# Kernel tuning notes

Measured on AMD Instinct MI355X. Metric: run time of the kernel, lower is better.

The kernel has to match this reference:

```python
import jax, jax.numpy as jnp
import numpy as np

N_NODES = 100000
N_EDGES = 600000
IN_CH = 128
HID = 128


def setup_inputs() -> dict:
    key = jax.random.key(0)
    ks = jax.random.split(key, 8)
    x = jax.random.normal(ks[0], (N_NODES, IN_CH), dtype=jnp.float32)
    edge_index = jax.random.randint(ks[1], (2, N_EDGES), 0, N_NODES, dtype=jnp.int64)
    # Linear weights stored as (in, out); scaled like torch default init
    W1 = jax.random.normal(ks[2], (2 * IN_CH, HID), dtype=jnp.float32) / np.sqrt(2 * IN_CH)
    b1 = jnp.zeros((HID,), dtype=jnp.float32)
    W2 = jax.random.normal(ks[3], (HID, HID), dtype=jnp.float32) / np.sqrt(HID)
    b2 = jnp.zeros((HID,), dtype=jnp.float32)
    W3 = jax.random.normal(ks[4], (HID, 1), dtype=jnp.float32) / np.sqrt(HID)
    b3 = jnp.zeros((1,), dtype=jnp.float32)
    return {"x": x, "edge_index": edge_index, "W1": W1, "b1": b1,
            "W2": W2, "b2": b2, "W3": W3, "b3": b3}


def reference(x, edge_index, W1, b1, W2, b2, W3, b3):
    src = edge_index[0]
    tgt = edge_index[1]
    # gather + concat: [n_edges, 2*in_channels]
    h = jnp.concatenate([x[src, :], x[tgt, :]], axis=1)
    h = jax.nn.elu(h @ W1 + b1)
    h = jax.nn.elu(h @ W2 + b2)
    h = h @ W3 + b3  # [n_edges, 1]
    return jnp.squeeze(h)  # squeeze=True path -> [n_edges]
```

## Files before the change

kernel.cpp:

```cpp
#include <hip/hip_runtime.h>

#define N_NODES 100000
#define N_EDGES 600000
#define NT1 1563
#define NT2 9375
#define LDH 136
typedef _Float16 f16x8 __attribute__((ext_vector_type(8)));
typedef __attribute__((ext_vector_type(4))) float f32x4;

__device__ __forceinline__ float elu_f(float v) {
    return v > 0.0f ? v : (__expf(v) - 1.0f);
}

extern "C" __global__ __launch_bounds__(256)
void k0_w1f(const float* __restrict__ W1, _Float16* __restrict__ W1f) {
    const int t = threadIdx.x;
    const int id = blockIdx.x * 256 + t;
    const int lane = id & 63, f = id >> 6;
    const int ks = f & 3, c = (f >> 2) & 1, half = (f >> 3) & 1, w = f >> 4;
    const int ln = lane & 15, kg = lane >> 4;
    const int col = w * 32 + c * 16 + ln;
    f16x8 v;
#pragma unroll
    for (int j = 0; j < 8; ++j)
        v[j] = (_Float16)W1[(half * 128 + ks * 32 + kg * 8 + j) * 128 + col];
    *(f16x8*)(W1f + (size_t)id * 8) = v;
}

extern "C" __global__ __launch_bounds__(256, 3)
void k1_node_linear(const float* __restrict__ x, const _Float16* __restrict__ W1f,
                    _Float16* __restrict__ P) {
    __shared__ __align__(16) _Float16 sX[64 * LDH];

    const int t = threadIdx.x;
    const int w = t >> 6, lane = t & 63;
    const int ln = lane & 15, kg = lane >> 4;
    const int le = t >> 2;
    const int q  = t & 3;

    f16x8 bf[2][2][4];
#pragma unroll
    for (int half = 0; half < 2; ++half)
#pragma unroll
        for (int c = 0; c < 2; ++c)
#pragma unroll
            for (int ks = 0; ks < 4; ++ks)
                bf[half][c][ks] = *(const f16x8*)(
                    W1f + (size_t)((w * 16 + half * 8 + c * 4 + ks) * 64 + lane) * 8);

    for (int tile = blockIdx.x; tile < NT1; tile += gridDim.x) {
        const int n0 = tile * 64;
        __syncthreads();

        {
            int n = n0 + le;
#pragma unroll
            for (int i = 0; i < 4; ++i) {
                float4 a0 = make_float4(0.f, 0.f, 0.f, 0.f), a1 = a0;
                if (n < N_NODES) {
                    const float* p = x + (size_t)n * 128 + q * 32 + i * 8;
                    a0 = *(const float4*)p; a1 = *(const float4*)(p + 4);
                }
                f16x8 vh;
                vh[0] = (_Float16)a0.x; vh[1] = (_Float16)a0.y;
                vh[2] = (_Float16)a0.z; vh[3] = (_Float16)a0.w;
                vh[4] = (_Float16)a1.x; vh[5] = (_Float16)a1.y;
                vh[6] = (_Float16)a1.z; vh[7] = (_Float16)a1.w;
                *(f16x8*)(&sX[le * LDH + q * 32 + i * 8]) = vh;
            }
        }
        __syncthreads();

        f32x4 acc[2][4][2];
#pragma unroll
        for (int half = 0; half < 2; ++half)
#pragma unroll
            for (int rt = 0; rt < 4; ++rt)
#pragma unroll
                for (int c = 0; c < 2; ++c) acc[half][rt][c] = (f32x4){0.f, 0.f, 0.f, 0.f};

#pragma unroll
        for (int ks = 0; ks < 4; ++ks) {
#pragma unroll
            for (int rt = 0; rt < 4; ++rt) {
                f16x8 a = *(const f16x8*)(&sX[(rt * 16 + ln) * LDH + ks * 32 + kg * 8]);
#pragma unroll
                for (int half = 0; half < 2; ++half)
#pragma unroll
                    for (int c = 0; c < 2; ++c)
                        acc[half][rt][c] = __builtin_amdgcn_mfma_f32_16x16x32_f16(
                            a, bf[half][c][ks], acc[half][rt][c], 0, 0, 0);
            }
        }

#pragma unroll
        for (int half = 0; half < 2; ++half) {
            __syncthreads();
#pragma unroll
            for (int rt = 0; rt < 4; ++rt)
#pragma unroll
                for (int c = 0; c < 2; ++c) {
                    int col = w * 32 + c * 16 + ln;
#pragma unroll
                    for (int reg = 0; reg < 4; ++reg) {
                        int row = rt * 16 + kg * 4 + reg;
                        sX[row * LDH + col] = (_Float16)acc[half][rt][c][reg];
                    }
                }
            __syncthreads();
            int n = n0 + le;
            if (n < N_NODES) {
                _Float16* dst = P + (size_t)n * 256 + half * 128 + q * 32;
                const _Float16* srcp = &sX[le * LDH + q * 32];
#pragma unroll
                for (int i = 0; i < 4; ++i)
                    *(f16x8*)(dst + i * 8) = *(const f16x8*)(srcp + i * 8);
            }
        }
    }
}

extern "C" __global__ __launch_bounds__(256, 3)
void k2_edge_mlp(const _Float16* __restrict__ P, const void* __restrict__ eiv,
                 const float* __restrict__ b1, const float* __restrict__ W2,
                 const float* __restrict__ b2, const float* __restrict__ W3,
                 const float* __restrict__ b3, float* __restrict__ out) {
    __shared__ __align__(16) _Float16 sH[2][64 * LDH];
    __shared__ float sPart[2][4][64];
    __shared__ int sFlag;

    const int t = threadIdx.x;
    const int w = t >> 6, lane = t & 63;
    const int ln = lane & 15, kg = lane >> 4;
    const int row = t >> 2;
    const int kc0 = (t & 3) * 4;
    const float b3v = b3[0];
    const int stride = gridDim.x;

    if (t < 64) {
        unsigned v = ((const unsigned*)eiv)[2 * t + 1];
        unsigned long long bm = __ballot(v == 0u);
        if (t == 0) sFlag = (bm == ~0ull) ? 1 : 0;
    }

    f16x8 b1f[4];
#pragma unroll
    for (int i = 0; i < 4; ++i)
#pragma unroll
        for (int j = 0; j < 8; ++j) b1f[i][j] = (_Float16)b1[(kc0 + i) * 8 + j];

    float w3v[2], b2v[2];
#pragma unroll
    for (int c = 0; c < 2; ++c) {
        int col = w * 32 + c * 16 + ln;
        w3v[c] = W3[col]; b2v[c] = b2[col];
    }

    f16x8 bfw[2][4];
#pragma unroll
    for (int c = 0; c < 2; ++c) {
        const int n = w * 32 + c * 16 + ln;
#pragma unroll
        for (int ks = 0; ks < 4; ++ks) {
            f16x8 v;
#pragma unroll
            for (int j = 0; j < 8; ++j) {
                int k = ks * 32 + kg * 8 + j;
                v[j] = (_Float16)W2[k * 128 + n];
            }
            bfw[c][ks] = v;
        }
    }
    __syncthreads();
    const int mode64 = sFlag;

    const int tile0 = blockIdx.x;

    int se_nx, ge_nx;
    {
        int e = tile0 * 64 + row;
        if (mode64) {
            se_nx = (int)((const long long*)eiv)[e];
            ge_nx = (int)((const long long*)eiv)[N_EDGES + e];
        } else {
            se_nx = ((const int*)eiv)[e];
            ge_nx = ((const int*)eiv)[N_EDGES + e];
        }
    }
    {
        const _Float16* pa = P + (size_t)se_nx * 256 + kc0 * 8;
        const _Float16* pb = P + (size_t)ge_nx * 256 + 128 + kc0 * 8;
        f16x8 Ga[4], Gb[4];
#pragma unroll
        for (int i = 0; i < 4; ++i) {
            Ga[i] = *(const f16x8*)(pa + i * 8);
            Gb[i] = *(const f16x8*)(pb + i * 8);
        }
#pragma unroll
        for (int i = 0; i < 4; ++i) {
            f16x8 s = Ga[i] + Gb[i] + b1f[i];
            f16x8 vh;
#pragma unroll
            for (int j = 0; j < 8; ++j) {
                _Float16 sv = s[j];
                vh[j] = (sv > (_Float16)0) ? sv
                        : (_Float16)(__expf((float)sv) - 1.0f);
            }
            *(f16x8*)(&sH[0][row * LDH + (kc0 + i) * 8]) = vh;
        }
    }
    {
        int t1 = tile0 + stride;
        int t1c = (t1 < NT2) ? t1 : tile0;
        int e = t1c * 64 + row;
        if (mode64) {
            se_nx = (int)((const long long*)eiv)[e];
            ge_nx = (int)((const long long*)eiv)[N_EDGES + e];
        } else {
            se_nx = ((const int*)eiv)[e];
            ge_nx = ((const int*)eiv)[N_EDGES + e];
        }
    }
    __syncthreads();

    int p = 0;
    int prevE0 = -1;
    for (int tile = tile0; tile < NT2; tile += stride) {
        const int nt = tile + stride;
        const int ntc = (nt < NT2) ? nt : tile;

        const _Float16* pa = P + (size_t)se_nx * 256 + kc0 * 8;
        const _Float16* pb = P + (size_t)ge_nx * 256 + 128 + kc0 * 8;
        f16x8 Ga[4], Gb[4];
#pragma unroll
        for (int i = 0; i < 4; ++i) {
            Ga[i] = *(const f16x8*)(pa + i * 8);
            Gb[i] = *(const f16x8*)(pb + i * 8);
        }

        {
            int n2 = nt + stride;
            int n2c = (n2 < NT2) ? n2 : ntc;
            int e = n2c * 64 + row;
            if (mode64) {
                se_nx = (int)((const long long*)eiv)[e];
                ge_nx = (int)((const long long*)eiv)[N_EDGES + e];
            } else {
                se_nx = ((const int*)eiv)[e];
                ge_nx = ((const int*)eiv)[N_EDGES + e];
            }
        }

        if (prevE0 >= 0 && t < 64)
            out[prevE0 + t] = sPart[p ^ 1][0][t] + sPart[p ^ 1][1][t] +
                              sPart[p ^ 1][2][t] + sPart[p ^ 1][3][t] + b3v;

        f32x4 acc[4][2];
#pragma unroll
        for (int rt = 0; rt < 4; ++rt)
#pragma unroll
            for (int c = 0; c < 2; ++c) acc[rt][c] = (f32x4){0.f, 0.f, 0.f, 0.f};

#pragma unroll
        for (int ks = 0; ks < 4; ++ks) {
#pragma unroll
            for (int rt = 0; rt < 4; ++rt) {
                f16x8 a = *(const f16x8*)(&sH[p][(rt * 16 + ln) * LDH + ks * 32 + kg * 8]);
#pragma unroll
                for (int c = 0; c < 2; ++c)
                    acc[rt][c] = __builtin_amdgcn_mfma_f32_16x16x32_f16(a, bfw[c][ks], acc[rt][c], 0, 0, 0);
            }
        }

#pragma unroll
        for (int rt = 0; rt < 4; ++rt) {
            float pr[4] = {0.f, 0.f, 0.f, 0.f};
#pragma unroll
            for (int c = 0; c < 2; ++c) {
#pragma unroll
                for (int reg = 0; reg < 4; ++reg)
                    pr[reg] += elu_f(acc[rt][c][reg] + b2v[c]) * w3v[c];
            }
#pragma unroll
            for (int m = 1; m < 16; m <<= 1)
#pragma unroll
                for (int reg = 0; reg < 4; ++reg) pr[reg] += __shfl_xor(pr[reg], m, 64);
            if (ln == 0) {
#pragma unroll
                for (int reg = 0; reg < 4; ++reg)
                    sPart[p][w][rt * 16 + kg * 4 + reg] = pr[reg];
            }
        }

#pragma unroll
        for (int i = 0; i < 4; ++i) {
            f16x8 s = Ga[i] + Gb[i] + b1f[i];
            f16x8 vh;
#pragma unroll
            for (int j = 0; j < 8; ++j) {
                _Float16 sv = s[j];
                vh[j] = (sv > (_Float16)0) ? sv
                        : (_Float16)(__expf((float)sv) - 1.0f);
            }
            *(f16x8*)(&sH[p ^ 1][row * LDH + (kc0 + i) * 8]) = vh;
        }

        prevE0 = tile * 64;
        __syncthreads();
        p ^= 1;
    }

    if (prevE0 >= 0 && t < 64)
        out[prevE0 + t] = sPart[p ^ 1][0][t] + sPart[p ^ 1][1][t] +
                          sPart[p ^ 1][2][t] + sPart[p ^ 1][3][t] + b3v;
}

extern "C" void kernel_launch(void* const* d_in, const int* in_sizes, int n_in,
                              void* d_out, int out_size, void* d_ws, size_t ws_size,
                              hipStream_t stream) {
    const float* x  = (const float*)d_in[0];
    const void*  ei = d_in[1];
    const float* W1 = (const float*)d_in[2];
    const float* b1 = (const float*)d_in[3];
    const float* W2 = (const float*)d_in[4];
    const float* b2 = (const float*)d_in[5];
    const float* W3 = (const float*)d_in[6];
    const float* b3 = (const float*)d_in[7];
    float* out = (float*)d_out;

    _Float16* P   = (_Float16*)((char*)d_ws + 256);
    _Float16* W1f = P + (size_t)N_NODES * 256;

    k0_w1f<<<16, 256, 0, stream>>>(W1, W1f);
    k1_node_linear<<<768, 256, 0, stream>>>(x, W1f, P);
    k2_edge_mlp<<<768, 256, 0, stream>>>(P, ei, b1, W2, b2, W3, b3, out);
}
```

Before: 192.1 us.

## Prefetch gathered node rows one tile ahead via register double buffer

Moves the gather of the source and target node rows for tile t+1 into iteration t, and loads edge indices two tiles ahead instead of one. The rows are held in a second register buffer and rotated at the end of each iteration. The aim is to hide the latency of the random global gathers behind the MFMA and ELU work of the current tile. In exchange it costs about 32 more VGPRs, which may lower occupancy. The prologue index loads for tile0+stride and tile0+2*stride are not clamped against the tile count.

New measurement: 240.0 us. 25.0% more time.

```diff
diff --git a/kernel.cpp b/kernel.cpp
--- a/kernel.cpp
+++ b/kernel.cpp
@@ -176,20 +176,22 @@
 
     const int tile0 = blockIdx.x;
 
-    int se_nx, ge_nx;
+#define LOAD_IDX(TT, SE, GE) do {                                   \
+        int e_ = (TT) * 64 + row;                                   \
+        if (mode64) {                                               \
+            SE = (int)((const long long*)eiv)[e_];                  \
+            GE = (int)((const long long*)eiv)[N_EDGES + e_];        \
+        } else {                                                    \
+            SE = ((const int*)eiv)[e_];                             \
+            GE = ((const int*)eiv)[N_EDGES + e_];                   \
+        }                                                           \
+    } while (0)
+
     {
-        int e = tile0 * 64 + row;
-        if (mode64) {
-            se_nx = (int)((const long long*)eiv)[e];
-            ge_nx = (int)((const long long*)eiv)[N_EDGES + e];
-        } else {
-            se_nx = ((const int*)eiv)[e];
-            ge_nx = ((const int*)eiv)[N_EDGES + e];
-        }
-    }
-    {
-        const _Float16* pa = P + (size_t)se_nx * 256 + kc0 * 8;
-        const _Float16* pb = P + (size_t)ge_nx * 256 + 128 + kc0 * 8;
+        int se, ge;
+        LOAD_IDX(tile0, se, ge);
+        const _Float16* pa = P + (size_t)se * 256 + kc0 * 8;
+        const _Float16* pb = P + (size_t)ge * 256 + 128 + kc0 * 8;
         f16x8 Ga[4], Gb[4];
 #pragma unroll
         for (int i = 0; i < 4; ++i) {
@@ -209,46 +211,40 @@
             *(f16x8*)(&sH[0][row * LDH + (kc0 + i) * 8]) = vh;
         }
     }
+    f16x8 GaA[4], GbA[4];
     {
-        int t1 = tile0 + stride;
-        int t1c = (t1 < NT2) ? t1 : tile0;
-        int e = t1c * 64 + row;
-        if (mode64) {
-            se_nx = (int)((const long long*)eiv)[e];
-            ge_nx = (int)((const long long*)eiv)[N_EDGES + e];
-        } else {
-            se_nx = ((const int*)eiv)[e];
-            ge_nx = ((const int*)eiv)[N_EDGES + e];
-        }
-    }
+        int se, ge;
+        LOAD_IDX(tile0 + stride, se, ge);
+        const _Float16* pa = P + (size_t)se * 256 + kc0 * 8;
+        const _Float16* pb = P + (size_t)ge * 256 + 128 + kc0 * 8;
+#pragma unroll
+        for (int i = 0; i < 4; ++i) {
+            GaA[i] = *(const f16x8*)(pa + i * 8);
+            GbA[i] = *(const f16x8*)(pb + i * 8);
+        }
+    }
+    int se_nx, ge_nx;
+    LOAD_IDX(tile0 + 2 * stride, se_nx, ge_nx);
     __syncthreads();
 
     int p = 0;
     int prevE0 = -1;
     for (int tile = tile0; tile < NT2; tile += stride) {
-        const int nt = tile + stride;
-        const int ntc = (nt < NT2) ? nt : tile;
-
-        const _Float16* pa = P + (size_t)se_nx * 256 + kc0 * 8;
-        const _Float16* pb = P + (size_t)ge_nx * 256 + 128 + kc0 * 8;
-        f16x8 Ga[4], Gb[4];
-#pragma unroll
-        for (int i = 0; i < 4; ++i) {
-            Ga[i] = *(const f16x8*)(pa + i * 8);
-            Gb[i] = *(const f16x8*)(pb + i * 8);
-        }
-
+        f16x8 GaB[4], GbB[4];
         {
-            int n2 = nt + stride;
-            int n2c = (n2 < NT2) ? n2 : ntc;
-            int e = n2c * 64 + row;
-            if (mode64) {
-                se_nx = (int)((const long long*)eiv)[e];
-                ge_nx = (int)((const long long*)eiv)[N_EDGES + e];
-            } else {
-                se_nx = ((const int*)eiv)[e];
-                ge_nx = ((const int*)eiv)[N_EDGES + e];
-            }
+            const _Float16* pa = P + (size_t)se_nx * 256 + kc0 * 8;
+            const _Float16* pb = P + (size_t)ge_nx * 256 + 128 + kc0 * 8;
+#pragma unroll
+            for (int i = 0; i < 4; ++i) {
+                GaB[i] = *(const f16x8*)(pa + i * 8);
+                GbB[i] = *(const f16x8*)(pb + i * 8);
+            }
+        }
+
+        {
+            int n3 = tile + 3 * stride;
+            int n3c = (n3 < NT2) ? n3 : tile;
+            LOAD_IDX(n3c, se_nx, ge_nx);
         }
 
         if (prevE0 >= 0 && t < 64)
@@ -294,7 +290,7 @@
 
 #pragma unroll
         for (int i = 0; i < 4; ++i) {
-            f16x8 s = Ga[i] + Gb[i] + b1f[i];
+            f16x8 s = GaA[i] + GbA[i] + b1f[i];
             f16x8 vh;
 #pragma unroll
             for (int j = 0; j < 8; ++j) {
@@ -305,6 +301,12 @@
             *(f16x8*)(&sH[p ^ 1][row * LDH + (kc0 + i) * 8]) = vh;
         }
 
+#pragma unroll
+        for (int i = 0; i < 4; ++i) {
+            GaA[i] = GaB[i];
+            GbA[i] = GbB[i];
+        }
+
         prevE0 = tile * 64;
         __syncthreads();
         p ^= 1;
@@ -313,6 +315,7 @@
     if (prevE0 >= 0 && t < 64)
         out[prevE0 + t] = sPart[p ^ 1][0][t] + sPart[p ^ 1][1][t] +
                           sPart[p ^ 1][2][t] + sPart[p ^ 1][3][t] + b3v;
+#undef LOAD_IDX
 }
 
 extern "C" void kernel_launch(void* const* d_in, const int* in_sizes, int n_in,
```

## Bucket-sort edges by source node block to improve gather locality

Applied to the files above, without the earlier changes.

Adds histogram, scan and scatter kernels that group edges by source node in blocks of 64, storing packed (src,tgt) pairs and the original edge index. The edge MLP then reads the sorted pairs and scatters each result back to its original position. This is meant to make the source-side gathers of P more cache-friendly. In exchange it adds three extra launches, atomics and a single-block scan, and output writes become scattered.

Result: slower. 379.4 us (+97.5%).

```diff
diff --git a/kernel.cpp b/kernel.cpp
--- a/kernel.cpp
+++ b/kernel.cpp
@@ -4,6 +4,7 @@
 #define N_EDGES 600000
 #define NT1 1563
 #define NT2 9375
+#define NB  1563
 #define LDH 136
 typedef _Float16 f16x8 __attribute__((ext_vector_type(8)));
 typedef __attribute__((ext_vector_type(4))) float f32x4;
@@ -12,10 +13,21 @@
     return v > 0.0f ? v : (__expf(v) - 1.0f);
 }
 
+#define DETECT_MODE(SFLAG, MODE)                                        \
+    if (threadIdx.x < 64) {                                             \
+        unsigned v_ = ((const unsigned*)eiv)[2 * threadIdx.x + 1];      \
+        unsigned long long bm_ = __ballot(v_ == 0u);                    \
+        if (threadIdx.x == 0) SFLAG = (bm_ == ~0ull) ? 1 : 0;           \
+    }                                                                   \
+    __syncthreads();                                                    \
+    const int MODE = SFLAG;
+
 extern "C" __global__ __launch_bounds__(256)
-void k0_w1f(const float* __restrict__ W1, _Float16* __restrict__ W1f) {
+void k0_w1f(const float* __restrict__ W1, _Float16* __restrict__ W1f,
+            int* __restrict__ cnt) {
     const int t = threadIdx.x;
     const int id = blockIdx.x * 256 + t;
+    if (id < NB) cnt[id] = 0;
     const int lane = id & 63, f = id >> 6;
     const int ks = f & 3, c = (f >> 2) & 1, half = (f >> 3) & 1, w = f >> 4;
     const int ln = lane & 15, kg = lane >> 4;
@@ -25,6 +37,63 @@
     for (int j = 0; j < 8; ++j)
         v[j] = (_Float16)W1[(half * 128 + ks * 32 + kg * 8 + j) * 128 + col];
     *(f16x8*)(W1f + (size_t)id * 8) = v;
+}
+
+extern "C" __global__ __launch_bounds__(256)
+void k_hist(const void* __restrict__ eiv, int* __restrict__ cnt) {
+    __shared__ int sFlag;
+    DETECT_MODE(sFlag, mode64)
+    const int step = gridDim.x * blockDim.x;
+    for (int e = blockIdx.x * blockDim.x + threadIdx.x; e < N_EDGES; e += step) {
+        int se = mode64 ? (int)((const long long*)eiv)[e] : ((const int*)eiv)[e];
+        atomicAdd(&cnt[se >> 6], 1);
+    }
+}
+
+extern "C" __global__ __launch_bounds__(256)
+void k_scan(const int* __restrict__ cnt, int* __restrict__ off) {
+    __shared__ int sSum[256];
+    const int t = threadIdx.x;
+    const int base = t * 7;
+    int loc[7]; int s = 0;
+#pragma unroll
+    for (int i = 0; i < 7; ++i) {
+        int idx = base + i;
+        int v = (idx < NB) ? cnt[idx] : 0;
+        loc[i] = s; s += v;
+    }
+    sSum[t] = s; __syncthreads();
+    for (int d = 1; d < 256; d <<= 1) {
+        int v = (t >= d) ? sSum[t - d] : 0;
+        __syncthreads();
+        sSum[t] += v;
+        __syncthreads();
+    }
+    int pre = sSum[t] - s;
+#pragma unroll
+    for (int i = 0; i < 7; ++i)
+        if (base + i < NB) off[base + i] = pre + loc[i];
+}
+
+extern "C" __global__ __launch_bounds__(256)
+void k_scatter(const void* __restrict__ eiv, int* __restrict__ off,
+               int2* __restrict__ ES, int* __restrict__ orig) {
+    __shared__ int sFlag;
+    DETECT_MODE(sFlag, mode64)
+    const int step = gridDim.x * blockDim.x;
+    for (int e = blockIdx.x * blockDim.x + threadIdx.x; e < N_EDGES; e += step) {
+        int se, ge;
+        if (mode64) {
+            se = (int)((const long long*)eiv)[e];
+            ge = (int)((const long long*)eiv)[N_EDGES + e];
+        } else {
+            se = ((const int*)eiv)[e];
+            ge = ((const int*)eiv)[N_EDGES + e];
+        }
+        int pos = atomicAdd(&off[se >> 6], 1);
+        ES[pos] = make_int2(se, ge);
+        orig[pos] = e;
+    }
 }
 
 extern "C" __global__ __launch_bounds__(256, 3)
@@ -121,13 +190,13 @@
 }
 
 extern "C" __global__ __launch_bounds__(256, 3)
-void k2_edge_mlp(const _Float16* __restrict__ P, const void* __restrict__ eiv,
+void k2_edge_mlp(const _Float16* __restrict__ P, const int2* __restrict__ ES,
+                 const int* __restrict__ orig,
                  const float* __restrict__ b1, const float* __restrict__ W2,
                  const float* __restrict__ b2, const float* __restrict__ W3,
                  const float* __restrict__ b3, float* __restrict__ out) {
     __shared__ __align__(16) _Float16 sH[2][64 * LDH];
     __shared__ float sPart[2][4][64];
-    __shared__ int sFlag;
 
     const int t = threadIdx.x;
     const int w = t >> 6, lane = t & 63;
@@ -137,12 +206,6 @@
     const float b3v = b3[0];
     const int stride = gridDim.x;
 
-    if (t < 64) {
-        unsigned v = ((const unsigned*)eiv)[2 * t + 1];
-        unsigned long long bm = __ballot(v == 0u);
-        if (t == 0) sFlag = (bm == ~0ull) ? 1 : 0;
-    }
-
     f16x8 b1f[4];
 #pragma unroll
     for (int i = 0; i < 4; ++i)
@@ -171,25 +234,14 @@
             bfw[c][ks] = v;
         }
     }
-    __syncthreads();
-    const int mode64 = sFlag;
 
     const int tile0 = blockIdx.x;
 
     int se_nx, ge_nx;
     {
-        int e = tile0 * 64 + row;
-        if (mode64) {
-            se_nx = (int)((const long long*)eiv)[e];
-            ge_nx = (int)((const long long*)eiv)[N_EDGES + e];
-        } else {
-            se_nx = ((const int*)eiv)[e];
-            ge_nx = ((const int*)eiv)[N_EDGES + e];
-        }
-    }
-    {
-        const _Float16* pa = P + (size_t)se_nx * 256 + kc0 * 8;
-        const _Float16* pb = P + (size_t)ge_nx * 256 + 128 + kc0 * 8;
+        int2 eg = ES[tile0 * 64 + row];
+        const _Float16* pa = P + (size_t)eg.x * 256 + kc0 * 8;
+        const _Float16* pb = P + (size_t)eg.y * 256 + 128 + kc0 * 8;
         f16x8 Ga[4], Gb[4];
 #pragma unroll
         for (int i = 0; i < 4; ++i) {
@@ -212,14 +264,8 @@
     {
         int t1 = tile0 + stride;
         int t1c = (t1 < NT2) ? t1 : tile0;
-        int e = t1c * 64 + row;
-        if (mode64) {
-            se_nx = (int)((const long long*)eiv)[e];
-            ge_nx = (int)((const long long*)eiv)[N_EDGES + e];
-        } else {
-            se_nx = ((const int*)eiv)[e];
-            ge_nx = ((const int*)eiv)[N_EDGES + e];
-        }
+        int2 eg = ES[t1c * 64 + row];
+        se_nx = eg.x; ge_nx = eg.y;
     }
     __syncthreads();
 
@@ -241,19 +287,15 @@
         {
             int n2 = nt + stride;
             int n2c = (n2 < NT2) ? n2 : ntc;
-            int e = n2c * 64 + row;
-            if (mode64) {
-                se_nx = (int)((const long long*)eiv)[e];
-                ge_nx = (int)((const long long*)eiv)[N_EDGES + e];
-            } else {
-                se_nx = ((const int*)eiv)[e];
-                ge_nx = ((const int*)eiv)[N_EDGES + e];
-            }
-        }
-
-        if (prevE0 >= 0 && t < 64)
-            out[prevE0 + t] = sPart[p ^ 1][0][t] + sPart[p ^ 1][1][t] +
-                              sPart[p ^ 1][2][t] + sPart[p ^ 1][3][t] + b3v;
+            int2 eg = ES[n2c * 64 + row];
+            se_nx = eg.x; ge_nx = eg.y;
+        }
+
+        if (prevE0 >= 0 && t < 64) {
+            int o = orig[prevE0 + t];
+            out[o] = sPart[p ^ 1][0][t] + sPart[p ^ 1][1][t] +
+                     sPart[p ^ 1][2][t] + sPart[p ^ 1][3][t] + b3v;
+        }
 
         f32x4 acc[4][2];
 #pragma unroll
@@ -310,9 +352,11 @@
         p ^= 1;
     }
 
-    if (prevE0 >= 0 && t < 64)
-        out[prevE0 + t] = sPart[p ^ 1][0][t] + sPart[p ^ 1][1][t] +
-                          sPart[p ^ 1][2][t] + sPart[p ^ 1][3][t] + b3v;
+    if (prevE0 >= 0 && t < 64) {
+        int o = orig[prevE0 + t];
+        out[o] = sPart[p ^ 1][0][t] + sPart[p ^ 1][1][t] +
+                 sPart[p ^ 1][2][t] + sPart[p ^ 1][3][t] + b3v;
+    }
 }
 
 extern "C" void kernel_launch(void* const* d_in, const int* in_sizes, int n_in,
@@ -328,10 +372,18 @@
     const float* b3 = (const float*)d_in[7];
     float* out = (float*)d_out;
 
-    _Float16* P   = (_Float16*)((char*)d_ws + 256);
-    _Float16* W1f = P + (size_t)N_NODES * 256;
-
-    k0_w1f<<<16, 256, 0, stream>>>(W1, W1f);
+    char* wsp = (char*)d_ws + 256;
+    _Float16* P    = (_Float16*)wsp;                   wsp += (size_t)N_NODES * 256 * 2;
+    _Float16* W1f  = (_Float16*)wsp;                   wsp += 4096 * 16;
+    int2*     ES   = (int2*)wsp;                       wsp += (size_t)N_EDGES * 8;
+    int*      orig = (int*)wsp;                        wsp += (size_t)N_EDGES * 4;
+    int*      cnt  = (int*)wsp;                        wsp += ((NB * 4 + 255) & ~255);
+    int*      off  = (int*)wsp;
+
+    k0_w1f<<<16, 256, 0, stream>>>(W1, W1f, cnt);
+    k_hist<<<1024, 256, 0, stream>>>(ei, cnt);
+    k_scan<<<1, 256, 0, stream>>>(cnt, off);
+    k_scatter<<<1024, 256, 0, stream>>>(ei, off, ES, orig);
     k1_node_linear<<<768, 256, 0, stream>>>(x, W1f, P);
-    k2_edge_mlp<<<768, 256, 0, stream>>>(P, ei, b1, W2, b2, W3, b3, out);
-}
+    k2_edge_mlp<<<768, 256, 0, stream>>>(P, ES, orig, b1, W2, b2, W3, b3, out);
+}
```
